# Kernel optimization log

Hardware: AMD Instinct MI355X
Metric: run time of the kernel (lower is better)

Reference implementation:

```python
import jax, jax.numpy as jnp
import numpy as np

B, N, IN, H, L, C = 2048, 100, 64, 256, 3, 3
NEG_SLOPE = 0.2


def setup_inputs() -> dict:
    key = jax.random.key(0)
    ks = jax.random.split(key, 11)
    s = lambda k, sh: jax.random.normal(k, sh, dtype=jnp.float32) * 0.05
    return {
        'x': jax.random.normal(ks[0], (B, N, IN), dtype=jnp.float32),
        'W_exp': s(ks[1], (IN, H)), 'b_exp': s(ks[2], (H,)),
        'W_l': s(ks[3], (L, H, H)), 'b_l': s(ks[4], (L, H)),
        'W_r': s(ks[5], (L, H, H)), 'b_r': s(ks[6], (L, H)),
        'att': s(ks[7], (L, H)), 'bias': s(ks[8], (L, H)),
        'W_fc': s(ks[9], (H, C)), 'b_fc': s(ks[10], (C,)),
    }


def _make_pe(n, d):
    pos = jnp.arange(n, dtype=jnp.float32)[:, None]
    div = jnp.exp(jnp.arange(0, d, 2, dtype=jnp.float32) * (-jnp.log(jnp.float32(10000.0)) / d))
    pe = jnp.zeros((n, d), dtype=jnp.float32)
    pe = pe.at[:, 0::2].set(jnp.sin(pos * div))
    pe = pe.at[:, 1::2].set(jnp.cos(pos * div))
    return pe


def _edges(n):
    # bidirectional chain + self loops (GATv2Conv add_self_loops=True)
    src = np.concatenate([np.arange(n - 1), np.arange(1, n), np.arange(n)])
    dst = np.concatenate([np.arange(1, n), np.arange(n - 1), np.arange(n)])
    return jnp.asarray(src), jnp.asarray(dst)


def _gatv2_conv(x, src, dst, Wl, bl, Wr, br, a, b, n):
    # x: [B,N,H]; PyG GATv2Conv, heads=1, share_weights=False
    xl = x @ Wl + bl                      # source transform [B,N,H]
    xr = x @ Wr + br                      # target transform [B,N,H]
    m = jax.nn.leaky_relu(xl[:, src] + xr[:, dst], NEG_SLOPE)   # [B,E,H]
    logits = jnp.einsum('beh,h->be', m, a)                      # [B,E]
    seg_max = jax.vmap(lambda l: jax.ops.segment_max(l, dst, num_segments=n))(logits)
    ex = jnp.exp(logits - seg_max[:, dst])
    denom = jax.vmap(lambda e: jax.ops.segment_sum(e, dst, num_segments=n))(ex)
    alpha = ex / denom[:, dst]                                  # [B,E]
    msgs = alpha[:, :, None] * xl[:, src]                       # [B,E,H]
    out = jax.vmap(lambda mm: jax.ops.segment_sum(mm, dst, num_segments=n))(msgs)
    return out + b


def reference(x, W_exp, b_exp, W_l, b_l, W_r, b_r, att, bias, W_fc, b_fc):
    n = x.shape[1]
    src, dst = _edges(n)
    x0 = x @ W_exp + b_exp + _make_pe(n, W_exp.shape[1])   # expander + positional encoding
    # Faithful to original: the loop feeds batch.x (= x0) into every conv layer,
    # so the output of the loop is the LAST conv applied to x0.
    h = x0
    for l in range(W_l.shape[0]):
        h = _gatv2_conv(x0, src, dst, W_l[l], b_l[l], W_r[l], b_r[l], att[l], bias[l], n)
    pooled = h.sum(axis=1)                                 # global_add_pool -> [B,H]
    return pooled @ W_fc + b_fc                            # [B,num_classes]
```

## Files before the change

kernel.cpp:

```cpp
#include <hip/hip_runtime.h>
#include <hip/hip_bf16.h>

#define BB 2048
#define NN 100
#define INF_ 64
#define HH 256
#define CC 3

typedef __attribute__((ext_vector_type(8))) short s8v;
typedef __attribute__((ext_vector_type(4))) float f4v;

static __device__ __forceinline__ unsigned short f2bf(float f) {
    union { float f; unsigned int u; } c; c.f = f;
    unsigned int r = c.u + 0x7FFF + ((c.u >> 16) & 1);
    return (unsigned short)(r >> 16);
}
static __device__ __forceinline__ unsigned int pk2(float lo, float hi) {
    return (unsigned int)f2bf(lo) | ((unsigned int)f2bf(hi) << 16);
}
static __device__ __forceinline__ float u2f_lo(unsigned int u) {
    union { float f; unsigned int i; } c; c.i = u << 16; return c.f;
}
static __device__ __forceinline__ float u2f_hi(unsigned int u) {
    union { float f; unsigned int i; } c; c.i = u & 0xffff0000u; return c.f;
}
static __device__ __forceinline__ int swzA(int row, int col) {
    return (row * HH + col) ^ ((row & 7) << 3);
}

__global__ __launch_bounds__(256) void precompute_k(
    const float* __restrict__ W_exp, const float* __restrict__ b_exp,
    const float* __restrict__ W_l, const float* __restrict__ b_l,
    const float* __restrict__ W_r, const float* __restrict__ b_r,
    float* __restrict__ Wcomb, float* __restrict__ cadd)
{
    int r = blockIdx.x;
    int z = blockIdx.y;
    int t = threadIdx.x;
    const float* Wg = (z ? W_r : W_l) + 2 * HH * HH;
    const float* bg = (z ? b_r : b_l) + 2 * HH;

    __shared__ float sa[HH];
    float a;
    if (r < INF_) {
        a = W_exp[r * HH + t];
    } else {
        int n = r - INF_;
        float div = expf((float)(t & 254) * (-0.03597789207803f));
        float ang = (float)n * div;
        a = b_exp[t] + ((t & 1) ? cosf(ang) : sinf(ang));
    }
    sa[t] = a;
    __syncthreads();

    float acc = 0.f;
    #pragma unroll 8
    for (int h = 0; h < HH; ++h)
        acc += sa[h] * Wg[h * HH + t];

    if (r < INF_) Wcomb[(z * INF_ + r) * HH + t] = acc;
    else          cadd[(z * NN + (r - INF_)) * HH + t] = acc + bg[t];
}

#define N_WF 32768
#define N_CF4 14336

__global__ __launch_bounds__(256) void rearrange_k(
    const float* __restrict__ Wcomb, const float* __restrict__ cadd,
    unsigned short* __restrict__ WF, float* __restrict__ CFf)
{
    int i = blockIdx.x * 256 + threadIdx.x;
    if (i < N_WF) {
        int j = i & 7, lane = (i >> 3) & 63, ks = (i >> 9) & 1;
        int nt = (i >> 10) & 15, z = (i >> 14) & 1;
        int k = ks * 32 + 4 * (lane >> 4) + (j & 3) + 16 * (j >> 2);
        int n = nt * 16 + (lane & 15);
        WF[i] = f2bf(Wcomb[(z * INF_ + k) * HH + n]);
    } else if (i < N_WF + N_CF4) {
        int i2 = i - N_WF;
        int lane = i2 & 63, nt = (i2 >> 6) & 15;
        int zm = i2 >> 10;
        int mt = zm % 7, z = zm / 7;
        int node = mt * 16 + (lane & 15);
        int feat = nt * 16 + (lane >> 4) * 4;
        float4 v = {0.f, 0.f, 0.f, 0.f};
        if (node < NN)
            v = *(const float4*)&cadd[(z * NN + node) * HH + feat];
        *(float4*)&CFf[(size_t)i2 * 4] = v;
    }
}

__global__ __launch_bounds__(512, 4) void fused_k(
    const float* __restrict__ x,
    const unsigned short* __restrict__ WF, const float* __restrict__ CFf,
    const float* __restrict__ att, const float* __restrict__ bias,
    const float* __restrict__ Wfc, const float* __restrict__ bfc,
    float* __restrict__ out)
{
    __shared__ unsigned short sxl[NN * HH];
    __shared__ unsigned short sxr[NN * 64];
    __shared__ unsigned short sxs[896 * 8];
    __shared__ float satt[HH];

    int b = blockIdx.x, t = threadIdx.x;
    int wave = t >> 6, lane = t & 63, g = lane >> 4, li = lane & 15;

    if (t < HH) satt[t] = att[2 * HH + t];

    const float* xb = x + (size_t)b * (NN * INF_);
    for (int s = t; s < 896; s += 512) {
        int sl = s & 63, ks = (s >> 6) & 1, mt = s >> 7;
        int m = mt * 16 + (sl & 15), gg = sl >> 4;
        union { s8v v; unsigned int u[4]; } a;
        if (m < NN) {
            float4 u = *(const float4*)&xb[m * INF_ + ks * 32 + 4 * gg];
            float4 v = *(const float4*)&xb[m * INF_ + ks * 32 + 16 + 4 * gg];
            a.u[0] = pk2(u.x, u.y);
            a.u[1] = pk2(u.z, u.w);
            a.u[2] = pk2(v.x, v.y);
            a.u[3] = pk2(v.z, v.w);
        } else {
            a.u[0] = a.u[1] = a.u[2] = a.u[3] = 0u;
        }
        *(s8v*)&sxs[s * 8] = a.v;
    }

    int q8 = t >> 3, c8 = (t & 7) * 8;
    int eBL[5], eBR[5];
    bool eva[5];
    float pv[5], pa[5];
    #pragma unroll
    for (int i = 0; i < 5; ++i) {
        int e = q8 + 64 * i;
        bool inr = (e < 300);
        int es = inr ? (e / 3) : 0;
        int ed = es + (e - 3 * es) - 1;
        bool v = inr && ed >= 0 && ed < NN;
        eva[i] = v;
        int dd = v ? ed : 0;
        eBL[i] = 2 * (es * HH + (c8 ^ ((es & 7) << 3)));
        eBR[i] = 2 * (dd * 64 + (c8 ^ ((dd & 7) << 3)));
        pv[i] = 0.f; pa[i] = 0.f;
    }

    int z = wave >> 2;
    int ntw = wave & 3;
    __syncthreads();

    #pragma unroll
    for (int q = 0; q < 4; ++q) {
        int nt = q * 4 + ntw;
        const s8v* bp = (const s8v*)WF + (size_t)(z * 16 + nt) * 2 * 64;
        s8v w0 = bp[lane];
        s8v w1 = bp[64 + lane];
        const s8v* sp = (const s8v*)sxs;
        unsigned short* dstp = z ? sxr : sxl;
        int colbase = (z ? (ntw * 16) : (nt * 16)) + g * 4;
        int rowstride = z ? 64 : HH;
        #pragma unroll
        for (int mt = 0; mt < 7; ++mt) {
            f4v c = *(const f4v*)&CFf[((size_t)((z * 7 + mt) * 16 + nt) * 64 + lane) * 4];
            s8v a0 = sp[mt * 128 + lane];
            s8v a1 = sp[mt * 128 + 64 + lane];
            c = __builtin_amdgcn_mfma_f32_16x16x32_bf16(w0, a0, c, 0, 0, 0);
            c = __builtin_amdgcn_mfma_f32_16x16x32_bf16(w1, a1, c, 0, 0, 0);
            int node = mt * 16 + li;
            if (mt < 6 || li < 4) {
                unsigned int lo = pk2(c[0], c[1]);
                unsigned int hi = pk2(c[2], c[3]);
                int elem = (node * rowstride + colbase) ^ ((li & 7) << 3);
                uint2 wv2 = { lo, hi };
                *(uint2*)&dstp[elem] = wv2;
            }
        }
        __syncthreads();

        float4 at0 = *(const float4*)&satt[q * 64 + c8];
        float4 at1 = *(const float4*)&satt[q * 64 + c8 + 4];
        #pragma unroll
        for (int i = 0; i < 5; ++i) {
            if (eva[i]) {
                uint4 ua = *(const uint4*)((const char*)sxl + (eBL[i] + q * 128));
                uint4 ub = *(const uint4*)((const char*)sxr + eBR[i]);
                float fv, fa;
                #define PROC(UL, UR, A0, A1) { \
                    float v0 = u2f_lo(UL) + u2f_lo(UR); \
                    float v1 = u2f_hi(UL) + u2f_hi(UR); \
                    fv = fmaf(A0, v0, fv); fa = fmaf(A0, fabsf(v0), fa); \
                    fv = fmaf(A1, v1, fv); fa = fmaf(A1, fabsf(v1), fa); }
                fv = 0.f; fa = 0.f;
                PROC(ua.x, ub.x, at0.x, at0.y);
                PROC(ua.y, ub.y, at0.z, at0.w);
                PROC(ua.z, ub.z, at1.x, at1.y);
                PROC(ua.w, ub.w, at1.z, at1.w);
                #undef PROC
                pv[i] += fv; pa[i] += fa;
            }
        }
        __syncthreads();
    }

    float* lg      = (float*)sxs;
    float* wvp     = lg + 304;
    float* partial = wvp + 104;

    #pragma unroll
    for (int i = 0; i < 5; ++i) {
        float s = fmaf(0.6f, pv[i], 0.4f * pa[i]);
        s += __shfl_xor(s, 1, 64);
        s += __shfl_xor(s, 2, 64);
        s += __shfl_xor(s, 4, 64);
        int e = q8 + 64 * i;
        if ((t & 7) == 0 && e < 300)
            lg[e] = eva[i] ? s : -1e30f;
    }
    __syncthreads();

    if (t < NN) {
        int i = t;
        float w = 0.f;
        #pragma unroll
        for (int dj = -1; dj <= 1; ++dj) {
            int j = i + dj;
            if (j < 0 || j >= NN) continue;
            float l0 = (j - 1 >= 0) ? lg[3 * (j - 1) + 2] : -1e30f;
            float l1 = lg[3 * j + 1];
            float l2 = (j + 1 < NN) ? lg[3 * (j + 1) + 0] : -1e30f;
            float mx = fmaxf(fmaxf(l0, l1), l2);
            float den = expf(l0 - mx) + expf(l1 - mx) + expf(l2 - mx);
            float myl = lg[3 * i + dj + 1];
            w += expf(myl - mx) / den;
        }
        wvp[i] = w;
    }
    __syncthreads();

    {
        float pa0 = 0.f, pa1 = 0.f, pa2 = 0.f, pa3 = 0.f;
        int r0 = wave * 13;
        int r1 = (r0 + 13 < NN) ? r0 + 13 : NN;
        int c0 = lane * 4;
        for (int row = r0; row < r1; ++row) {
            float wr = wvp[row];
            uint2 u = *(const uint2*)&sxl[swzA(row, c0)];
            pa0 = fmaf(wr, u2f_lo(u.x), pa0);
            pa1 = fmaf(wr, u2f_hi(u.x), pa1);
            pa2 = fmaf(wr, u2f_lo(u.y), pa2);
            pa3 = fmaf(wr, u2f_hi(u.y), pa3);
        }
        float* pp = (float*)sxr;
        float4 pvv = { pa0, pa1, pa2, pa3 };
        *(float4*)&pp[wave * HH + c0] = pvv;
    }
    __syncthreads();

    if (t < HH) {
        const float* pp = (const float*)sxr;
        float pooled = 100.f * bias[2 * HH + t];
        #pragma unroll
        for (int w = 0; w < 8; ++w) pooled += pp[w * HH + t];

        float p0 = pooled * Wfc[t * 3 + 0];
        float p1 = pooled * Wfc[t * 3 + 1];
        float p2 = pooled * Wfc[t * 3 + 2];
        #pragma unroll
        for (int off = 32; off; off >>= 1) {
            p0 += __shfl_down(p0, off, 64);
            p1 += __shfl_down(p1, off, 64);
            p2 += __shfl_down(p2, off, 64);
        }
        if (lane == 0) {
            partial[wave * 3 + 0] = p0;
            partial[wave * 3 + 1] = p1;
            partial[wave * 3 + 2] = p2;
        }
    }
    __syncthreads();
    if (t < CC) {
        out[(size_t)b * CC + t] =
            partial[0 * 3 + t] + partial[1 * 3 + t] +
            partial[2 * 3 + t] + partial[3 * 3 + t] + bfc[t];
    }
}

extern "C" void kernel_launch(void* const* d_in, const int* in_sizes, int n_in,
                              void* d_out, int out_size, void* d_ws, size_t ws_size,
                              hipStream_t stream) {
    const float* x     = (const float*)d_in[0];
    const float* W_exp = (const float*)d_in[1];
    const float* b_exp = (const float*)d_in[2];
    const float* W_l   = (const float*)d_in[3];
    const float* b_l   = (const float*)d_in[4];
    const float* W_r   = (const float*)d_in[5];
    const float* b_r   = (const float*)d_in[6];
    const float* att   = (const float*)d_in[7];
    const float* bias  = (const float*)d_in[8];
    const float* W_fc  = (const float*)d_in[9];
    const float* b_fc  = (const float*)d_in[10];
    float* out = (float*)d_out;

    char* ws = (char*)d_ws;
    float* Wcomb = (float*)ws;
    float* cadd  = (float*)(ws + 131072);
    unsigned short* WF = (unsigned short*)(ws + 131072 + 204800);
    float* CFf = (float*)(ws + 131072 + 204800 + 65536);

    precompute_k<<<dim3(164, 2), 256, 0, stream>>>(W_exp, b_exp, W_l, b_l, W_r, b_r,
                                                   Wcomb, cadd);
    rearrange_k<<<184, 256, 0, stream>>>(Wcomb, cadd, WF, CFf);
    fused_k<<<BB, 512, 0, stream>>>(x, WF, CFf, att, bias, W_fc, b_fc, out);
}
```

Measured before the change: 83.54 us.

## Pool via input-space weighted sum instead of storing full xl tile in LDS

The change drops the full 100x256 bf16 xl buffer from shared memory and keeps only the 64-column slice used for each chunk's attention logits. The pooled output is rebuilt algebraically: attention weights are applied to the raw 64-wide input rows, and the result is multiplied by the combined weight matrix plus a weighted sum of the constant-add rows, all read from global memory. Shared memory drops from about 65 KB to about 28 KB per block, and launch bounds are raised to allow 8 blocks per CU for higher occupancy. In exchange, each block issues extra global reads of Wcomb and cadd (about 164 rows of 256 floats) and a serial per-thread dot-product loop in the epilogue. Pooling is now done in fp32 rather than from bf16-rounded xl.

Measured after the change: 88.51 us. 1.06x slower.

```diff
diff --git a/kernel.cpp b/kernel.cpp
--- a/kernel.cpp
+++ b/kernel.cpp
@@ -23,9 +23,6 @@
 }
 static __device__ __forceinline__ float u2f_hi(unsigned int u) {
     union { float f; unsigned int i; } c; c.i = u & 0xffff0000u; return c.f;
-}
-static __device__ __forceinline__ int swzA(int row, int col) {
-    return (row * HH + col) ^ ((row & 7) << 3);
 }
 
 __global__ __launch_bounds__(256) void precompute_k(
@@ -90,14 +87,15 @@
     }
 }
 
-__global__ __launch_bounds__(512, 4) void fused_k(
+__global__ __launch_bounds__(512, 8) void fused_k(
     const float* __restrict__ x,
     const unsigned short* __restrict__ WF, const float* __restrict__ CFf,
+    const float* __restrict__ Wcomb, const float* __restrict__ cadd,
     const float* __restrict__ att, const float* __restrict__ bias,
     const float* __restrict__ Wfc, const float* __restrict__ bfc,
     float* __restrict__ out)
 {
-    __shared__ unsigned short sxl[NN * HH];
+    __shared__ unsigned short sxl[NN * 64];
     __shared__ unsigned short sxr[NN * 64];
     __shared__ unsigned short sxs[896 * 8];
     __shared__ float satt[HH];
@@ -138,7 +136,7 @@
         bool v = inr && ed >= 0 && ed < NN;
         eva[i] = v;
         int dd = v ? ed : 0;
-        eBL[i] = 2 * (es * HH + (c8 ^ ((es & 7) << 3)));
+        eBL[i] = 2 * (es * 64 + (c8 ^ ((es & 7) << 3)));
         eBR[i] = 2 * (dd * 64 + (c8 ^ ((dd & 7) << 3)));
         pv[i] = 0.f; pa[i] = 0.f;
     }
@@ -155,8 +153,7 @@
         s8v w1 = bp[64 + lane];
         const s8v* sp = (const s8v*)sxs;
         unsigned short* dstp = z ? sxr : sxl;
-        int colbase = (z ? (ntw * 16) : (nt * 16)) + g * 4;
-        int rowstride = z ? 64 : HH;
+        int colbase = ntw * 16 + g * 4;
         #pragma unroll
         for (int mt = 0; mt < 7; ++mt) {
             f4v c = *(const f4v*)&CFf[((size_t)((z * 7 + mt) * 16 + nt) * 64 + lane) * 4];
@@ -168,7 +165,7 @@
             if (mt < 6 || li < 4) {
                 unsigned int lo = pk2(c[0], c[1]);
                 unsigned int hi = pk2(c[2], c[3]);
-                int elem = (node * rowstride + colbase) ^ ((li & 7) << 3);
+                int elem = node * 64 + (colbase ^ ((li & 7) << 3));
                 uint2 wv2 = { lo, hi };
                 *(uint2*)&dstp[elem] = wv2;
             }
@@ -180,7 +177,7 @@
         #pragma unroll
         for (int i = 0; i < 5; ++i) {
             if (eva[i]) {
-                uint4 ua = *(const uint4*)((const char*)sxl + (eBL[i] + q * 128));
+                uint4 ua = *(const uint4*)((const char*)sxl + eBL[i]);
                 uint4 ub = *(const uint4*)((const char*)sxr + eBR[i]);
                 float fv, fa;
                 #define PROC(UL, UR, A0, A1) { \
@@ -203,6 +200,7 @@
     float* lg      = (float*)sxs;
     float* wvp     = lg + 304;
     float* partial = wvp + 104;
+    float* ypart   = partial + 16;
 
     #pragma unroll
     for (int i = 0; i < 5; ++i) {
@@ -236,33 +234,34 @@
     __syncthreads();
 
     {
-        float pa0 = 0.f, pa1 = 0.f, pa2 = 0.f, pa3 = 0.f;
         int r0 = wave * 13;
         int r1 = (r0 + 13 < NN) ? r0 + 13 : NN;
-        int c0 = lane * 4;
-        for (int row = r0; row < r1; ++row) {
-            float wr = wvp[row];
-            uint2 u = *(const uint2*)&sxl[swzA(row, c0)];
-            pa0 = fmaf(wr, u2f_lo(u.x), pa0);
-            pa1 = fmaf(wr, u2f_hi(u.x), pa1);
-            pa2 = fmaf(wr, u2f_lo(u.y), pa2);
-            pa3 = fmaf(wr, u2f_hi(u.y), pa3);
-        }
-        float* pp = (float*)sxr;
-        float4 pvv = { pa0, pa1, pa2, pa3 };
-        *(float4*)&pp[wave * HH + c0] = pvv;
+        float acc = 0.f;
+        for (int i = r0; i < r1; ++i)
+            acc = fmaf(wvp[i], xb[i * INF_ + lane], acc);
+        ypart[wave * 64 + lane] = acc;
+    }
+    __syncthreads();
+    if (t < 64) {
+        float s = 0.f;
+        #pragma unroll
+        for (int w = 0; w < 8; ++w) s += ypart[w * 64 + t];
+        ypart[t] = s;
     }
     __syncthreads();
 
     if (t < HH) {
-        const float* pp = (const float*)sxr;
-        float pooled = 100.f * bias[2 * HH + t];
-        #pragma unroll
-        for (int w = 0; w < 8; ++w) pooled += pp[w * HH + t];
-
-        float p0 = pooled * Wfc[t * 3 + 0];
-        float p1 = pooled * Wfc[t * 3 + 1];
-        float p2 = pooled * Wfc[t * 3 + 2];
+        float p = 100.f * bias[2 * HH + t];
+        #pragma unroll 8
+        for (int k = 0; k < INF_; ++k)
+            p = fmaf(ypart[k], Wcomb[k * HH + t], p);
+        #pragma unroll 4
+        for (int i = 0; i < NN; ++i)
+            p = fmaf(wvp[i], cadd[i * HH + t], p);
+
+        float p0 = p * Wfc[t * 3 + 0];
+        float p1 = p * Wfc[t * 3 + 1];
+        float p2 = p * Wfc[t * 3 + 2];
         #pragma unroll
         for (int off = 32; off; off >>= 1) {
             p0 += __shfl_down(p0, off, 64);
@@ -308,5 +307,5 @@
     precompute_k<<<dim3(164, 2), 256, 0, stream>>>(W_exp, b_exp, W_l, b_l, W_r, b_r,
                                                    Wcomb, cadd);
     rearrange_k<<<184, 256, 0, stream>>>(Wcomb, cadd, WF, CFf);
-    fused_k<<<BB, 512, 0, stream>>>(x, WF, CFf, att, bias, W_fc, b_fc, out);
-}
+    fused_k<<<BB, 512, 0, stream>>>(x, WF, CFf, Wcomb, cadd, att, bias, W_fc, b_fc, out);
+}
```
